# Optimization experiments

Hardware: AMD Instinct MI355X
Metric: run time of the kernel (lower is better)

## Reference

```python
import jax, jax.numpy as jnp
import numpy as np

B, N, M, D = 8, 4096, 1024, 256  # batch, query points, keys per batch, feature dim


def setup_inputs() -> dict:
    key = jax.random.key(0)
    ks = jax.random.split(key, 6)
    s = 1.0 / np.sqrt(D)
    p = jax.random.normal(ks[0], (B, N, 1, D), dtype=jnp.float32)
    r = jax.random.normal(ks[1], (B * M, D), dtype=jnp.float32)
    batch = jnp.repeat(jnp.arange(B, dtype=jnp.int64), M)  # sorted batch ids, batch[-1]=B-1
    Wh = jax.random.normal(ks[2], (D, D), dtype=jnp.float32) * s
    Wl = jax.random.normal(ks[3], (D, D), dtype=jnp.float32) * s
    Wg = jax.random.normal(ks[4], (D, D), dtype=jnp.float32) * s
    bh = jnp.zeros((D,), jnp.float32)
    bl = jnp.zeros((D,), jnp.float32)
    bg = jnp.zeros((D,), jnp.float32)
    return {"p": p, "r": r, "batch": batch, "Wh": Wh, "bh": bh,
            "Wl": Wl, "bl": bl, "Wg": Wg, "bg": bg}


def reference(p, r, batch, Wh, bh, Wl, bl, Wg, bg):
    # p: [B, N, 1, Dp]; r: [B*M, Dr] -> [B, M, Dr] (torch reshape with B = batch[-1]+1)
    Bsz = p.shape[0]
    r3 = r.reshape(Bsz, -1, r.shape[-1])              # [B, M, Dr]
    h = p[:, :, 0, :] @ Wh + bh                       # [B, N, D]   (mlp_h)
    l = r3 @ Wl + bl                                  # [B, M, D]   (mlp_l)
    # broadcasted inner-product score (torch: expand/unsqueeze/matmul/squeeze)
    scores = jnp.einsum('bnd,bmd->bnm', h, l)         # [B, N, M]
    attn = jax.nn.softmax(scores, axis=-1)            # softmax over M
    g = r3 @ Wg + bg                                  # [B, M, Dg]  (mlp_g)
    out = p[:, :, 0, :] + jnp.einsum('bnm,bmd->bnd', attn, g)  # [B, N, Dg]
    return out
```

## Files before the change

kernel.cpp:

```cpp
#include <hip/hip_runtime.h>
#include <hip/hip_fp16.h>

typedef short s16x8 __attribute__((ext_vector_type(8)));
typedef float f32x4 __attribute__((ext_vector_type(4)));
typedef float f32x16 __attribute__((ext_vector_type(16)));
typedef unsigned short u16;

static __device__ __forceinline__ u16 f2bf(float f) {
  union { float f; unsigned u; } c; c.f = f;
  unsigned u = c.u;
  u += 0x7FFFu + ((u >> 16) & 1u);
  return (u16)(u >> 16);
}
static __device__ __forceinline__ u16 f2h(float f) {
  return __half_as_ushort(__float2half(f));
}
static __device__ __forceinline__ int cvtpk_bf16(float a, float b) {
  int r;
  asm("v_cvt_pk_bf16_f32 %0, %1, %2" : "=v"(r) : "v"(a), "v"(b));
  return r;
}

static __device__ __forceinline__ void dma16(const u16* g, u16* l) {
  __builtin_amdgcn_global_load_lds(
      (const __attribute__((address_space(1))) unsigned int*)g,
      (__attribute__((address_space(3))) unsigned int*)l, 16, 0, 0);
}

__global__ __launch_bounds__(256) void wsplit_kernel(
    const float* __restrict__ Wh, const float* __restrict__ Wl,
    const float* __restrict__ Wg,
    u16* __restrict__ wh_sw, u16* __restrict__ wl_sw, u16* __restrict__ wg_sw) {
  int n = blockIdx.x, k = threadIdx.x, w = blockIdx.y;
  const float* W = (w == 0) ? Wh : (w == 1) ? Wl : Wg;
  u16* T = (w == 0) ? wh_sw : (w == 1) ? wl_sw : wg_sw;
  int ks = k >> 5, q = (k >> 3) & 3, j = k & 7;
  T[ks * 8192 + n * 32 + ((q ^ ((n >> 1) & 3))) * 8 + j] = f2h(W[k * 256 + n]);
}

__global__ __launch_bounds__(256, 3) void gemm1p_kernel(
    const float* __restrict__ p, const float* __restrict__ r,
    const u16* __restrict__ wh_sw, const u16* __restrict__ wl_sw,
    const u16* __restrict__ wg_sw,
    const float* __restrict__ bh, const float* __restrict__ bl,
    const float* __restrict__ bg,
    u16* __restrict__ h16, u16* __restrict__ l_sw, u16* __restrict__ g_sw) {
  __shared__ __align__(16) u16 wtile[2][8192];
  const int wave = threadIdx.x >> 6;
  const int lane = threadIdx.x & 63;
  const int quad = lane >> 4;
  const int l16  = lane & 15;
  const int bid  = blockIdx.x;

  const float* X; const u16* wsw; const float* bias; int mode, row0;
  if (bid < 512) {
    X = p; wsw = wh_sw; bias = bh; mode = 0; row0 = bid * 64 + wave * 16;
  } else if (bid < 640) {
    X = r; wsw = wl_sw; bias = bl; mode = 1; row0 = (bid - 512) * 64 + wave * 16;
  } else {
    X = r; wsw = wg_sw; bias = bg; mode = 2; row0 = (bid - 640) * 64 + wave * 16;
  }

  {
    const u16* src = wsw + wave * 2048 + lane * 8;
    u16* dst = &wtile[0][wave * 2048];
#pragma unroll
    for (int i = 0; i < 4; ++i) dma16(src + i * 512, dst + i * 512);
  }

  s16x8 a[8];
  {
    const float* xr = X + (size_t)(row0 + l16) * 256 + quad * 8;
#pragma unroll
    for (int ks = 0; ks < 8; ++ks) {
      f32x4 f0 = *(const f32x4*)(xr + ks * 32);
      f32x4 f1 = *(const f32x4*)(xr + ks * 32 + 4);
#pragma unroll
      for (int j = 0; j < 4; ++j) {
        a[ks][j]     = (short)f2h(f0[j]);
        a[ks][j + 4] = (short)f2h(f1[j]);
      }
    }
  }

  f32x4 acc[16];
  const f32x4 fz = {0.f, 0.f, 0.f, 0.f};
#pragma unroll
  for (int i = 0; i < 16; ++i) acc[i] = fz;

  for (int ks = 0; ks < 8; ++ks) {
    const int cur = ks & 1;
    asm volatile("s_waitcnt vmcnt(0)\n\ts_barrier" ::: "memory");
    if (ks < 7) {
      const u16* src = wsw + (ks + 1) * 8192 + wave * 2048 + lane * 8;
      u16* dst = &wtile[cur ^ 1][wave * 2048];
#pragma unroll
      for (int i = 0; i < 4; ++i) dma16(src + i * 512, dst + i * 512);
    }
    const u16* wt = &wtile[cur][0];
#pragma unroll
    for (int nt = 0; nt < 16; ++nt) {
      const int n = nt * 16 + l16;
      s16x8 bf = *(const s16x8*)(wt + n * 32 + ((quad ^ ((n >> 1) & 3))) * 8);
      acc[nt] = __builtin_amdgcn_mfma_f32_16x16x32_f16(a[ks], bf, acc[nt], 0, 0, 0);
    }
  }

  __syncthreads();
  u16* stg = &wtile[0][0] + wave * 4096;

  const int batch = row0 >> 10;
  const int wdw   = (row0 & 1023) >> 5;
  const int mbase = row0 & 31;

  if (mode != 2) {
#pragma unroll
    for (int nt = 0; nt < 16; ++nt) {
      float bv = bias[nt * 16 + l16];
#pragma unroll
      for (int reg = 0; reg < 4; ++reg)
        stg[(quad * 4 + reg) * 256 + nt * 16 + l16] = f2h(acc[nt][reg] + bv);
    }
    if (mode == 0) {
#pragma unroll
      for (int it = 0; it < 8; ++it) {
        int off = it * 512 + lane * 8;
        *(s16x8*)(h16 + (size_t)row0 * 256 + off) = *(const s16x8*)(stg + off);
      }
    } else {
      u16* tb = l_sw + ((size_t)(batch * 32 + wdw)) * 8192;
#pragma unroll
      for (int it = 0; it < 8; ++it) {
        int off = it * 512 + lane * 8;
        int rr = off >> 8;
        int c = (off & 255) >> 3;
        int mw = mbase + rr;
        *(s16x8*)(tb + mw * 256 + ((c ^ mw)) * 8) = *(const s16x8*)(stg + off);
      }
    }
  } else {
#pragma unroll
    for (int nt = 0; nt < 16; ++nt) {
      float bv = bias[nt * 16 + l16];
#pragma unroll
      for (int reg = 0; reg < 4; ++reg)
        stg[(quad * 4 + reg) * 256 + nt * 16 + l16] = f2bf(acc[nt][reg] + bv);
    }
    u16* tb = g_sw + ((size_t)(batch * 32 + wdw)) * 8192;
    const int mc0 = mbase >> 3;
#pragma unroll
    for (int it = 0; it < 4; ++it) {
      int d = it * 64 + lane;
      s16x8 v0, v1;
#pragma unroll
      for (int i = 0; i < 8; ++i) v0[i] = (short)stg[i * 256 + d];
#pragma unroll
      for (int i = 0; i < 8; ++i) v1[i] = (short)stg[(i + 8) * 256 + d];
      int sw = (d >> 1) & 3;
      *(s16x8*)(tb + d * 32 + ((mc0 ^ sw)) * 8) = v0;
      *(s16x8*)(tb + d * 32 + (((mc0 + 1) ^ sw)) * 8) = v1;
    }
  }
}

__global__ __launch_bounds__(256, 1) void attn_kernel(
    const float* __restrict__ P,
    const u16* __restrict__ h16,
    const u16* __restrict__ l_sw, const u16* __restrict__ g_sw,
    float* __restrict__ out) {
  __shared__ __align__(16) u16 tiles[3][16384];
  const int wave = threadIdx.x >> 6;
  const int lane = threadIdx.x & 63;
  const int hi   = lane >> 5;
  const int dlo  = lane & 31;
  const int b    = blockIdx.x & 7;
  const int n0w  = (blockIdx.x >> 3) * 128 + wave * 32;

  const u16* lsw_b = l_sw + (size_t)b * 32 * 8192;
  const u16* gsw_b = g_sw + (size_t)b * 32 * 8192;

  s16x8 a[16];
  {
    const u16* hh = h16 + ((size_t)(b * 4096 + n0w + dlo)) * 256 + hi * 8;
#pragma unroll
    for (int s = 0; s < 16; ++s) a[s] = *(const s16x8*)(hh + s * 16);
  }
  asm volatile("s_waitcnt vmcnt(0)" ::: "memory");

  f32x16 oacc[8];
#pragma unroll
  for (int i = 0; i < 8; ++i)
#pragma unroll
    for (int j = 0; j < 16; ++j) oacc[i][j] = 0.f;
  float lsum = 0.f;

  const u16* dsrc = ((wave < 2) ? lsw_b : gsw_b) + (wave & 1) * 4096 + lane * 8;

#pragma unroll
  for (int t = 0; t < 2; ++t) {
    const u16* src = dsrc + t * 8192;
    u16* dst = &tiles[t][wave * 4096];
#pragma unroll
    for (int i = 0; i < 8; ++i) dma16(src + i * 512, dst + i * 512);
  }

  for (int w = 0; w < 32; ++w) {
    if (w < 31) asm volatile("s_waitcnt vmcnt(8)" ::: "memory");
    else        asm volatile("s_waitcnt vmcnt(0)" ::: "memory");
    asm volatile("s_barrier" ::: "memory");
    if (w + 2 < 32) {
      const u16* src = dsrc + (size_t)(w + 2) * 8192;
      u16* dst = &tiles[(w + 2) % 3][wave * 4096];
#pragma unroll
      for (int i = 0; i < 8; ++i) dma16(src + i * 512, dst + i * 512);
    }
    const u16* lt = &tiles[w % 3][0];
    const u16* gt = &tiles[w % 3][8192];

    f32x16 se, so;
#pragma unroll
    for (int j = 0; j < 16; ++j) { se[j] = 0.f; so[j] = 0.f; }
    const int rowb = dlo * 256;
    __builtin_amdgcn_s_setprio(1);
#pragma unroll
    for (int s = 0; s < 16; s += 2) {
      const int c0 = (s << 1) + hi;
      const int c1 = ((s + 1) << 1) + hi;
      s16x8 lf0 = *(const s16x8*)(lt + rowb + ((c0 ^ dlo) & 31) * 8);
      s16x8 lf1 = *(const s16x8*)(lt + rowb + ((c1 ^ dlo) & 31) * 8);
      se = __builtin_amdgcn_mfma_f32_32x32x16_f16(lf0, a[s],     se, 0, 0, 0);
      so = __builtin_amdgcn_mfma_f32_32x32x16_f16(lf1, a[s + 1], so, 0, 0, 0);
    }
    __builtin_amdgcn_s_setprio(0);

    float e[16];
#pragma unroll
    for (int r = 0; r < 16; ++r) {
      e[r] = __expf(se[r] + so[r] - 48.f);
      lsum += e[r];
    }
    int c[8];
#pragma unroll
    for (int i = 0; i < 8; ++i) c[i] = cvtpk_bf16(e[2 * i], e[2 * i + 1]);

    union { int i[4]; s16x8 v; } pa0, pa1;
    {
      int s0 = __shfl_xor(c[0], 32, 64);
      int s1 = __shfl_xor(c[1], 32, 64);
      int s2 = __shfl_xor(c[2], 32, 64);
      int s3 = __shfl_xor(c[3], 32, 64);
      pa0.i[0] = hi ? s2 : c[0];
      pa0.i[1] = hi ? s3 : c[1];
      pa0.i[2] = hi ? c[2] : s0;
      pa0.i[3] = hi ? c[3] : s1;
      int s4 = __shfl_xor(c[4], 32, 64);
      int s5 = __shfl_xor(c[5], 32, 64);
      int s6 = __shfl_xor(c[6], 32, 64);
      int s7 = __shfl_xor(c[7], 32, 64);
      pa1.i[0] = hi ? s6 : c[4];
      pa1.i[1] = hi ? s7 : c[5];
      pa1.i[2] = hi ? c[6] : s4;
      pa1.i[3] = hi ? c[7] : s5;
    }

    __builtin_amdgcn_s_setprio(1);
#pragma unroll
    for (int dt = 0; dt < 8; ++dt) {
      const int d = dt * 32 + dlo;
      const int sw = (d >> 1) & 3;
      const u16* gp = gt + d * 32;
      s16x8 g0 = *(const s16x8*)(gp + ((hi ^ sw)) * 8);
      s16x8 g1 = *(const s16x8*)(gp + (((2 + hi) ^ sw)) * 8);
      oacc[dt] = __builtin_amdgcn_mfma_f32_32x32x16_bf16(pa0.v, g0, oacc[dt], 0, 0, 0);
      oacc[dt] = __builtin_amdgcn_mfma_f32_32x32x16_bf16(pa1.v, g1, oacc[dt], 0, 0, 0);
    }
    __builtin_amdgcn_s_setprio(0);
  }

  float den  = lsum + __shfl_xor(lsum, 32, 64);
  float invd = 1.0f / den;
  const size_t nb = (size_t)b * 4096 + n0w;
#pragma unroll
  for (int r = 0; r < 16; ++r) {
    const int q = (r & 3) + 8 * (r >> 2) + 4 * hi;
    const float iv = __shfl(invd, q, 64);
    const size_t rowoff = (nb + q) * 256 + dlo;
#pragma unroll
    for (int dt = 0; dt < 8; ++dt) {
      size_t idx = rowoff + dt * 32;
      out[idx] = P[idx] + oacc[dt][r] * iv;
    }
  }
}

extern "C" void kernel_launch(void* const* d_in, const int* in_sizes, int n_in,
                              void* d_out, int out_size, void* d_ws, size_t ws_size,
                              hipStream_t stream) {
  const float* p  = (const float*)d_in[0];
  const float* r  = (const float*)d_in[1];
  const float* Wh = (const float*)d_in[3];
  const float* bh = (const float*)d_in[4];
  const float* Wl = (const float*)d_in[5];
  const float* bl = (const float*)d_in[6];
  const float* Wg = (const float*)d_in[7];
  const float* bg = (const float*)d_in[8];
  float* out = (float*)d_out;

  char* ws = (char*)d_ws;
  size_t off = 0;
  auto alloc = [&](size_t nbytes) -> void* {
    void* q = ws + off;
    off += (nbytes + 255) & ~(size_t)255;
    return q;
  };
  u16* wh_sw = (u16*)alloc(65536 * 2);
  u16* wl_sw = (u16*)alloc(65536 * 2);
  u16* wg_sw = (u16*)alloc(65536 * 2);
  u16* h16   = (u16*)alloc((size_t)32768 * 256 * 2);
  u16* l_swb = (u16*)alloc((size_t)8 * 32 * 8192 * 2);
  u16* g_swb = (u16*)alloc((size_t)8 * 32 * 8192 * 2);
  (void)ws_size; (void)in_sizes; (void)n_in; (void)out_size;

  wsplit_kernel<<<dim3(256, 3), 256, 0, stream>>>(Wh, Wl, Wg, wh_sw, wl_sw, wg_sw);
  gemm1p_kernel<<<768, 256, 0, stream>>>(
      p, r, wh_sw, wl_sw, wg_sw, bh, bl, bg, h16, l_swb, g_swb);
  attn_kernel<<<256, 256, 0, stream>>>(p, h16, l_swb, g_swb, out);
}
```

Measured before the change: 172.1 us.

## Split attention key loop across two wave groups and reduce partials in LDS

The attention block grows from 256 to 512 threads. Two groups of four waves each process half of the 32 key/value tiles for the same 128 queries, each group with its own double-buffered LDS staging. At the end, the second group writes its partial output accumulators and softmax denominators to LDS, and the first group combines them before writing. The goal is twice the waves per CU to hide MFMA and LDS latency on the otherwise one-wave-per-SIMD kernel. In exchange, staging drops from triple buffering with partial waits to double buffering with a full vmcnt wait, uses more LDS, and adds an LDS reduction epilogue.

```diff
diff --git a/kernel.cpp b/kernel.cpp
--- a/kernel.cpp
+++ b/kernel.cpp
@@ -163,25 +163,28 @@
   }
 }
 
-__global__ __launch_bounds__(256, 1) void attn_kernel(
+__global__ __launch_bounds__(512, 2) void attn_kernel(
     const float* __restrict__ P,
     const u16* __restrict__ h16,
     const u16* __restrict__ l_sw, const u16* __restrict__ g_sw,
     float* __restrict__ out) {
-  __shared__ __align__(16) u16 tiles[3][16384];
+  __shared__ __align__(16) u16 tiles[2][2][16384];
+  __shared__ float dpart[4][32];
   const int wave = threadIdx.x >> 6;
   const int lane = threadIdx.x & 63;
   const int hi   = lane >> 5;
   const int dlo  = lane & 31;
+  const int qt   = wave & 3;
+  const int kh   = wave >> 2;
   const int b    = blockIdx.x & 7;
-  const int n0w  = (blockIdx.x >> 3) * 128 + wave * 32;
+  const int n0   = (blockIdx.x >> 3) * 128 + qt * 32;
 
   const u16* lsw_b = l_sw + (size_t)b * 32 * 8192;
   const u16* gsw_b = g_sw + (size_t)b * 32 * 8192;
 
   s16x8 a[16];
   {
-    const u16* hh = h16 + ((size_t)(b * 4096 + n0w + dlo)) * 256 + hi * 8;
+    const u16* hh = h16 + ((size_t)(b * 4096 + n0 + dlo)) * 256 + hi * 8;
 #pragma unroll
     for (int s = 0; s < 16; ++s) a[s] = *(const s16x8*)(hh + s * 16);
   }
@@ -194,28 +197,23 @@
     for (int j = 0; j < 16; ++j) oacc[i][j] = 0.f;
   float lsum = 0.f;
 
-  const u16* dsrc = ((wave < 2) ? lsw_b : gsw_b) + (wave & 1) * 4096 + lane * 8;
-
-#pragma unroll
-  for (int t = 0; t < 2; ++t) {
-    const u16* src = dsrc + t * 8192;
-    u16* dst = &tiles[t][wave * 4096];
-#pragma unroll
-    for (int i = 0; i < 8; ++i) dma16(src + i * 512, dst + i * 512);
-  }
-
-  for (int w = 0; w < 32; ++w) {
-    if (w < 31) asm volatile("s_waitcnt vmcnt(8)" ::: "memory");
-    else        asm volatile("s_waitcnt vmcnt(0)" ::: "memory");
-    asm volatile("s_barrier" ::: "memory");
-    if (w + 2 < 32) {
-      const u16* src = dsrc + (size_t)(w + 2) * 8192;
-      u16* dst = &tiles[(w + 2) % 3][wave * 4096];
+  const u16* dsrc = ((qt < 2) ? lsw_b : gsw_b) + (size_t)kh * 16 * 8192 +
+                    (qt & 1) * 4096 + lane * 8;
+  u16* ldst = &tiles[kh][0][(qt < 2 ? 0 : 8192) + (qt & 1) * 4096];
+
+#pragma unroll
+  for (int i = 0; i < 8; ++i) dma16(dsrc + i * 512, ldst + i * 512);
+
+  for (int it = 0; it < 16; ++it) {
+    asm volatile("s_waitcnt vmcnt(0)\n\ts_barrier" ::: "memory");
+    if (it + 1 < 16) {
+      const u16* src = dsrc + (size_t)(it + 1) * 8192;
+      u16* dst = ldst + ((it + 1) & 1) * 16384;
 #pragma unroll
       for (int i = 0; i < 8; ++i) dma16(src + i * 512, dst + i * 512);
     }
-    const u16* lt = &tiles[w % 3][0];
-    const u16* gt = &tiles[w % 3][8192];
+    const u16* lt = &tiles[kh][it & 1][0];
+    const u16* gt = lt + 8192;
 
     f32x16 se, so;
 #pragma unroll
@@ -277,18 +275,34 @@
     __builtin_amdgcn_s_setprio(0);
   }
 
-  float den  = lsum + __shfl_xor(lsum, 32, 64);
-  float invd = 1.0f / den;
-  const size_t nb = (size_t)b * 4096 + n0w;
-#pragma unroll
-  for (int r = 0; r < 16; ++r) {
-    const int q = (r & 3) + 8 * (r >> 2) + 4 * hi;
-    const float iv = __shfl(invd, q, 64);
-    const size_t rowoff = (nb + q) * 256 + dlo;
-#pragma unroll
-    for (int dt = 0; dt < 8; ++dt) {
-      size_t idx = rowoff + dt * 32;
-      out[idx] = P[idx] + oacc[dt][r] * iv;
+  float denp = lsum + __shfl_xor(lsum, 32, 64);
+  __syncthreads();
+  float* obuf = (float*)&tiles[0][0][0];
+  float* ob = obuf + qt * 8192;
+  if (kh == 1) {
+#pragma unroll
+    for (int dt = 0; dt < 8; ++dt)
+#pragma unroll
+      for (int r = 0; r < 16; ++r) {
+        const int q = (r & 3) + 8 * (r >> 2) + 4 * hi;
+        ob[q * 256 + dt * 32 + dlo] = oacc[dt][r];
+      }
+    if (lane < 32) dpart[qt][lane] = denp;
+  }
+  __syncthreads();
+  if (kh == 0) {
+    const float invd = 1.0f / (denp + dpart[qt][dlo]);
+    const size_t nb = (size_t)b * 4096 + n0;
+#pragma unroll
+    for (int r = 0; r < 16; ++r) {
+      const int q = (r & 3) + 8 * (r >> 2) + 4 * hi;
+      const float iv = __shfl(invd, q, 64);
+      const size_t rowoff = (nb + q) * 256 + dlo;
+#pragma unroll
+      for (int dt = 0; dt < 8; ++dt) {
+        size_t idx = rowoff + dt * 32;
+        out[idx] = P[idx] + (oacc[dt][r] + ob[q * 256 + dt * 32 + dlo]) * iv;
+      }
     }
   }
 }
@@ -324,5 +338,5 @@
   wsplit_kernel<<<dim3(256, 3), 256, 0, stream>>>(Wh, Wl, Wg, wh_sw, wl_sw, wg_sw);
   gemm1p_kernel<<<768, 256, 0, stream>>>(
       p, r, wh_sw, wl_sw, wg_sw, bh, bl, bg, h16, l_swb, g_swb);
-  attn_kernel<<<256, 256, 0, stream>>>(p, h16, l_swb, g_swb, out);
-}
+  attn_kernel<<<256, 512, 0, stream>>>(p, h16, l_swb, g_swb, out);
+}
```

Result: faster. 167.3 us (-2.8%).
